# Kernel optimization log

Measured on AMD Instinct MI355X. Metric: run time of the kernel, lower is better.

The kernel has to match this reference:

```python
import jax, jax.numpy as jnp
import numpy as np


def setup_inputs() -> dict:
    key = jax.random.key(0)
    ks = jax.random.split(key, 13)
    B, T, D, H, E, C, S = 256, 64, 512, 512, 256, 6624, 26
    s = 0.05
    return {
        "batch_H": jax.random.normal(ks[0], (B, T, D), jnp.float32),
        "text": jax.random.randint(ks[1], (B, S), 0, C, jnp.int64),
        "W_i2h": jax.random.normal(ks[2], (H, D), jnp.float32) * s,
        "W_h2h": jax.random.normal(ks[3], (H, H), jnp.float32) * s,
        "b_h2h": jax.random.normal(ks[4], (H,), jnp.float32) * s,
        "w_score": jax.random.normal(ks[5], (H,), jnp.float32) * s,
        "W_ih": jax.random.normal(ks[6], (4 * H, D + E), jnp.float32) * s,
        "W_hh": jax.random.normal(ks[7], (4 * H, H), jnp.float32) * s,
        "b_ih": jax.random.normal(ks[8], (4 * H,), jnp.float32) * s,
        "b_hh": jax.random.normal(ks[9], (4 * H,), jnp.float32) * s,
        "emb": jax.random.normal(ks[10], (C, E), jnp.float32) * s,
        "W_gen": jax.random.normal(ks[11], (C, H), jnp.float32) * s,
        "b_gen": jax.random.normal(ks[12], (C,), jnp.float32) * s,
        "max_label_length": 25,
    }


def reference(batch_H, text, W_i2h, W_h2h, b_h2h, w_score, W_ih, W_hh,
              b_ih, b_hh, emb, W_gen, b_gen, max_label_length):
    B, T, D = batch_H.shape
    H = W_h2h.shape[0]
    num_steps = max_label_length + 1

    # i2h(batch_H) is constant across steps -> hoist out of the recurrence
    Hproj = jnp.einsum('btd,hd->bth', batch_H, W_i2h)  # [B,T,H]
    char_embs = emb[text[:, :num_steps]]               # [B,S,E]
    xs = jnp.transpose(char_embs, (1, 0, 2))           # [S,B,E]

    def step(carry, ce):
        h, c = carry
        hp = h @ W_h2h.T + b_h2h                       # [B,H]
        e = jnp.tanh(Hproj + hp[:, None, :]) @ w_score  # [B,T]
        alpha = jax.nn.softmax(e, axis=1)
        context = jnp.einsum('bt,btd->bd', alpha, batch_H)  # [B,D]
        x = jnp.concatenate([context, ce], axis=1)     # [B,D+E]
        gates = x @ W_ih.T + b_ih + h @ W_hh.T + b_hh  # [B,4H]
        i, f, g, o = jnp.split(gates, 4, axis=1)
        c_new = jax.nn.sigmoid(f) * c + jax.nn.sigmoid(i) * jnp.tanh(g)
        h_new = jax.nn.sigmoid(o) * jnp.tanh(c_new)
        return (h_new, c_new), h_new

    h0 = jnp.zeros((B, H), batch_H.dtype)
    c0 = jnp.zeros((B, H), batch_H.dtype)
    _, hs = jax.lax.scan(step, (h0, c0), xs)           # hs: [S,B,H]
    output_hiddens = jnp.transpose(hs, (1, 0, 2))      # [B,S,H]
    probs = output_hiddens @ W_gen.T + b_gen           # [B,S,C]
    return probs
```

## Files before the change

### kernel.cpp

```cpp
#include <hip/hip_runtime.h>

typedef unsigned short u16;
typedef unsigned int   u32;
typedef __attribute__((ext_vector_type(4))) float f32x4;
typedef __attribute__((ext_vector_type(8))) u16   u16x8;
typedef __attribute__((ext_vector_type(4))) u16   u16x4;
typedef __attribute__((ext_vector_type(4))) u32   u32x4;

__device__ __forceinline__ u16 f2bf(float x) {
  u32 u = __builtin_bit_cast(u32, x);
  u = (u + 0x7fffu + ((u >> 16) & 1u)) >> 16;
  return (u16)u;
}
__device__ __forceinline__ float bf2f(u16 h) {
  return __builtin_bit_cast(float, (u32)h << 16);
}
__device__ __forceinline__ float fast_sig(float x) { return 1.f / (1.f + __expf(-x)); }
__device__ __forceinline__ float fast_tanh(float x) {
  float e = __expf(2.f * x);
  return 1.f - 2.f / (e + 1.f);
}

__device__ __forceinline__ f32x4 mfma_bf16(u16x8 a, u16x8 b, f32x4 c) {
  asm volatile("v_mfma_f32_16x16x32_bf16 %0, %1, %2, %0" : "+v"(c) : "v"(a), "v"(b));
  return c;
}

__device__ __forceinline__ void gload_lds16(const void* g, void* l) {
  __builtin_amdgcn_global_load_lds(
      (__attribute__((address_space(1))) u32*)g,
      (__attribute__((address_space(3))) u32*)l, 16, 0, 0);
}

__device__ __forceinline__ void conv4(const float* __restrict__ s, u16* __restrict__ d, int i) {
  f32x4 v = *(const f32x4*)(s + i);
  u16x4 o;
  o.x = f2bf(v.x); o.y = f2bf(v.y); o.z = f2bf(v.z); o.w = f2bf(v.w);
  *(u16x4*)(d + i) = o;
}

__global__ __launch_bounds__(256) void k_prep(
    const float* __restrict__ batch_H, const float* __restrict__ W_i2h,
    const float* __restrict__ emb, const float* __restrict__ W_ih,
    const float* __restrict__ W_h2h, const float* __restrict__ W_hh,
    const float* __restrict__ W_gen, const float* __restrict__ b_ih,
    const float* __restrict__ b_hh,
    u16* __restrict__ bHb, u16* __restrict__ Wi2hb, u16* __restrict__ embb,
    u16* __restrict__ Wihb, u16* __restrict__ Whcatb, u16* __restrict__ Wgenb,
    float* __restrict__ biascat, u16* __restrict__ Acat, float* __restrict__ cst) {
  const u32 u = blockIdx.x * 256 + threadIdx.x;
  if (u < 2097152u) { conv4(batch_H, bHb, u * 4); return; }
  if (u < 2162688u) { conv4(W_i2h, Wi2hb, (u - 2097152u) * 4); return; }
  if (u < 2586624u) { conv4(emb, embb, (u - 2162688u) * 4); return; }
  if (u < 2979840u) { conv4(W_ih, Wihb, (u - 2586624u) * 4); return; }
  if (u < 3307520u) {
    int i = (u - 2979840u) * 4;
    int r = i >> 9, c = i & 511;
    const float* src = (r < 512) ? (W_h2h + (size_t)r * 512 + c)
                                 : (W_hh + (size_t)(r - 512) * 512 + c);
    f32x4 v = *(const f32x4*)src;
    u16x4 o;
    o.x = f2bf(v.x); o.y = f2bf(v.y); o.z = f2bf(v.z); o.w = f2bf(v.w);
    *(u16x4*)(Whcatb + i) = o;
    return;
  }
  if (u < 4159488u) {
    int i = (u - 3307520u) * 4;
    int r = i >> 9;
    if (r < 6624) conv4(W_gen, Wgenb, i);
    else *(u16x4*)(Wgenb + i) = (u16x4){0, 0, 0, 0};
    return;
  }
  if (u < 4160000u) {
    int j = (u - 4159488u) * 4;
    f32x4 a = *(const f32x4*)(b_ih + j), b = *(const f32x4*)(b_hh + j);
    f32x4 r = {a.x + b.x, a.y + b.y, a.z + b.z, a.w + b.w};
    *(f32x4*)(biascat + j) = r;
    return;
  }
  if (u < 4200960u) {
    *(u32x4*)((char*)Acat + (size_t)(u - 4160000u) * 16) = (u32x4){0, 0, 0, 0};
    return;
  }
  if (u < 4233728u) {
    *(u32x4*)((char*)cst + (size_t)(u - 4200960u) * 16) = (u32x4){0, 0, 0, 0};
    return;
  }
}

template <int BM, int BN, int WM, int WN, int OUT_MODE>
__global__ __launch_bounds__(256) void gemm_bt(const u16* __restrict__ A, int lda,
                                               const u16* __restrict__ B, int ldb,
                                               const float* __restrict__ bias,
                                               float* __restrict__ Cf, u16* __restrict__ Cb,
                                               int ldc, int Nreal, int K) {
  static_assert((BM / WM) * (BN / WN) == 4, "4 waves");
  constexpr int FM = WM / 16, FN = WN / 16;
  constexpr int NWC = BN / WN;
  constexpr int CHA = (BM * 4) / 256, CHB = (BN * 4) / 256;
  __shared__ __align__(16) u16 sA[BM * 32];
  __shared__ __align__(16) u16 sB[BN * 32];
  const int tid = threadIdx.x;
  const int lane = tid & 63, wave = tid >> 6;
  const int wr = wave / NWC, wc = wave % NWC;
  const int l15 = lane & 15, lhi = lane >> 4;
  const int m0 = blockIdx.y * BM, n0 = blockIdx.x * BN;

  f32x4 acc[FM][FN];
#pragma unroll
  for (int i = 0; i < FM; ++i)
#pragma unroll
    for (int j = 0; j < FN; ++j) acc[i][j] = 0.f;

  for (int k0 = 0; k0 < K; k0 += 32) {
    __syncthreads();
#pragma unroll
    for (int j = 0; j < CHA; ++j) {
      int idx = j * 256 + tid;
      int row = idx >> 2, cc = idx & 3;
      int c = cc ^ ((row >> 1) & 3);
      gload_lds16(A + (size_t)(m0 + row) * lda + (k0 + c * 8), sA + idx * 8);
    }
#pragma unroll
    for (int j = 0; j < CHB; ++j) {
      int idx = j * 256 + tid;
      int row = idx >> 2, cc = idx & 3;
      int c = cc ^ ((row >> 1) & 3);
      gload_lds16(B + (size_t)(n0 + row) * ldb + (k0 + c * 8), sB + idx * 8);
    }
    __syncthreads();

    u16x8 av[FM], bv[FN];
#pragma unroll
    for (int mi = 0; mi < FM; ++mi) {
      int row = wr * WM + mi * 16 + l15;
      int ch = row * 4 + (lhi ^ ((row >> 1) & 3));
      av[mi] = *(const u16x8*)(sA + ch * 8);
    }
#pragma unroll
    for (int ni = 0; ni < FN; ++ni) {
      int row = wc * WN + ni * 16 + l15;
      int ch = row * 4 + (lhi ^ ((row >> 1) & 3));
      bv[ni] = *(const u16x8*)(sB + ch * 8);
    }
#pragma unroll
    for (int mi = 0; mi < FM; ++mi)
#pragma unroll
      for (int ni = 0; ni < FN; ++ni) acc[mi][ni] = mfma_bf16(av[mi], bv[ni], acc[mi][ni]);
  }

  asm volatile("s_nop 7\ns_nop 7\ns_nop 7");

#pragma unroll
  for (int mi = 0; mi < FM; ++mi) {
#pragma unroll
    for (int ni = 0; ni < FN; ++ni) {
      int col = n0 + wc * WN + ni * 16 + l15;
      if (col < Nreal) {
        float bvv = (OUT_MODE == 1) ? bias[col] : 0.f;
#pragma unroll
        for (int r = 0; r < 4; ++r) {
          int row = m0 + wr * WM + mi * 16 + lhi * 4 + r;
          float v = acc[mi][ni][r] + bvv;
          if (OUT_MODE == 2)
            Cb[(size_t)row * ldc + col] = f2bf(v);
          else
            Cf[(size_t)row * ldc + col] = v;
        }
      }
    }
  }
}

__global__ __launch_bounds__(256) void kA_hpgh(const u16* __restrict__ Acat,
                                               const u16* __restrict__ Whcatb,
                                               const float* __restrict__ b_h2h,
                                               float* __restrict__ hpbuf,
                                               float* __restrict__ ghbuf) {
  __shared__ __align__(16) u16 sA[32 * 64];
  __shared__ __align__(16) u16 sB[128 * 64];
  const int tid = threadIdx.x;
  const int lane = tid & 63, wave = tid >> 6;
  const int wr = wave >> 1, wc = wave & 1;
  const int l15 = lane & 15, lhi = lane >> 4;
  const int b0 = ((int)blockIdx.x / 20) * 32, n0 = ((int)blockIdx.x % 20) * 128;

  f32x4 acc[4];
#pragma unroll
  for (int j = 0; j < 4; ++j) acc[j] = 0.f;

  for (int k0 = 0; k0 < 512; k0 += 64) {
    __syncthreads();
    {
      int row = tid >> 3, cc = tid & 7, c = cc ^ (row & 7);
      gload_lds16(Acat + (size_t)(b0 + row) * 1280 + 768 + k0 + c * 8, sA + tid * 8);
    }
#pragma unroll
    for (int j = 0; j < 4; ++j) {
      int idx = j * 256 + tid, row = idx >> 3, cc = idx & 7, c = cc ^ (row & 7);
      gload_lds16(Whcatb + (size_t)(n0 + row) * 512 + k0 + c * 8, sB + idx * 8);
    }
    __syncthreads();
#pragma unroll
    for (int ks = 0; ks < 2; ++ks) {
      u16x8 av, bv[4];
      {
        int row = wr * 16 + l15;
        int ch = row * 8 + ((ks * 4 + lhi) ^ (row & 7));
        av = *(const u16x8*)(sA + ch * 8);
      }
#pragma unroll
      for (int ni = 0; ni < 4; ++ni) {
        int row = wc * 64 + ni * 16 + l15;
        int ch = row * 8 + ((ks * 4 + lhi) ^ (row & 7));
        bv[ni] = *(const u16x8*)(sB + ch * 8);
      }
#pragma unroll
      for (int ni = 0; ni < 4; ++ni) acc[ni] = mfma_bf16(av, bv[ni], acc[ni]);
    }
  }
  asm volatile("s_nop 7\ns_nop 7\ns_nop 7");
#pragma unroll
  for (int ni = 0; ni < 4; ++ni) {
    int col = n0 + wc * 64 + ni * 16 + l15;
    int rowg = b0 + wr * 16 + lhi * 4;
    if (col < 512) {
      float bvv = b_h2h[col];
#pragma unroll
      for (int r = 0; r < 4; ++r)
        hpbuf[(size_t)(rowg + r) * 512 + col] = acc[ni][r] + bvv;
    } else {
#pragma unroll
      for (int r = 0; r < 4; ++r)
        ghbuf[(size_t)(rowg + r) * 2048 + col - 512] = acc[ni][r];
    }
  }
}

__global__ __launch_bounds__(256) void kB_attn(const u16* __restrict__ Hproj,
                                               const float* __restrict__ hpbuf,
                                               const float* __restrict__ wsc,
                                               const u16* __restrict__ bh,
                                               const u16* __restrict__ embb,
                                               const int* __restrict__ text, int step,
                                               u16* __restrict__ Acat) {
  const int b = blockIdx.x, tid = threadIdx.x;
  __shared__ float hpsp[528];
  __shared__ float wssp[528];
  __shared__ float es[64];

  {
    int j0 = tid * 2;
    hpsp[j0 + (j0 >> 5)] = hpbuf[(size_t)b * 512 + j0];
    hpsp[j0 + 1 + ((j0 + 1) >> 5)] = hpbuf[(size_t)b * 512 + j0 + 1];
    int pi = j0 + (j0 >> 5);
    wssp[pi] = wsc[j0];
    wssp[pi + 1] = wsc[j0 + 1];
  }
  __syncthreads();

  const int ch16 = tid & 15;
  const int hbase = ch16 * 33;
  const int hc = ch16 * 32;
  float hpr[32], wsr[32];
#pragma unroll
  for (int j = 0; j < 32; ++j) {
    hpr[j] = hpsp[hbase + j];
    wsr[j] = wssp[hbase + j];
  }
#pragma unroll
  for (int tg = 0; tg < 4; ++tg) {
    int t = tg * 16 + (tid >> 4);
    const u16* hr = Hproj + (size_t)(b * 64 + t) * 512 + hc;
    float s = 0.f;
#pragma unroll
    for (int jo = 0; jo < 32; jo += 8) {
      u16x8 hv = *(const u16x8*)(hr + jo);
#pragma unroll
      for (int j = 0; j < 8; ++j) {
        float x = bf2f(hv[j]) + hpr[jo + j];
        s += fast_tanh(x) * wsr[jo + j];
      }
    }
#pragma unroll
    for (int off = 8; off; off >>= 1) s += __shfl_xor(s, off, 16);
    if (ch16 == 0) es[t] = s;
  }
  __syncthreads();
  if (tid < 64) {
    float v = es[tid];
    float m = v;
#pragma unroll
    for (int o = 32; o; o >>= 1) m = fmaxf(m, __shfl_xor(m, o, 64));
    float p = __expf(v - m);
    float su = p;
#pragma unroll
    for (int o = 32; o; o >>= 1) su += __shfl_xor(su, o, 64);
    es[tid] = p / su;
  }
  __syncthreads();
  const u16* base = bh + (size_t)b * 32768 + tid * 2;
  float c0 = 0.f, c1 = 0.f;
#pragma unroll 8
  for (int t = 0; t < 64; ++t) {
    u32 w = *(const u32*)(base + t * 512);
    float a = es[t];
    c0 = fmaf(a, bf2f((u16)(w & 0xffffu)), c0);
    c1 = fmaf(a, bf2f((u16)(w >> 16)), c1);
  }
  u32 pk = (u32)f2bf(c0) | ((u32)f2bf(c1) << 16);
  *(u32*)(Acat + (size_t)b * 1280 + tid * 2) = pk;
  int ci = text[b * 26 + step];
  Acat[(size_t)b * 1280 + 512 + tid] = embb[(size_t)ci * 256 + tid];
}

__global__ __launch_bounds__(256) void kC_gates_lstm(const u16* __restrict__ Acat_ro,
                                                     const u16* __restrict__ Wihb,
                                                     const float* __restrict__ biascat,
                                                     const float* __restrict__ ghbuf,
                                                     float* __restrict__ cst,
                                                     u16* __restrict__ Acat,
                                                     u16* __restrict__ hsb, int step) {
  __shared__ __align__(16) char smem[20480];
  u16* sA = (u16*)smem;
  u16* sB = (u16*)(smem + 4096);
  const int tid = threadIdx.x;
  const int lane = tid & 63, wave = tid >> 6;
  const int wr = wave >> 1, wc = wave & 1;
  const int l15 = lane & 15, lhi = lane >> 4;
  const int jt = blockIdx.x;
  const int b0 = blockIdx.y * 32;

  f32x4 acc[4];
#pragma unroll
  for (int j = 0; j < 4; ++j) acc[j] = 0.f;

  for (int k0 = 0; k0 < 768; k0 += 64) {
    __syncthreads();
    {
      int row = tid >> 3, cc = tid & 7, c = cc ^ (row & 7);
      gload_lds16(Acat_ro + (size_t)(b0 + row) * 1280 + k0 + c * 8, sA + tid * 8);
    }
#pragma unroll
    for (int j = 0; j < 4; ++j) {
      int idx = j * 256 + tid, row = idx >> 3, cc = idx & 7, c = cc ^ (row & 7);
      int grow = (row >> 5) * 512 + jt * 32 + (row & 31);
      gload_lds16(Wihb + (size_t)grow * 768 + k0 + c * 8, sB + idx * 8);
    }
    __syncthreads();

#pragma unroll
    for (int ks = 0; ks < 2; ++ks) {
      u16x8 av, bv[4];
      {
        int row = wr * 16 + l15;
        int ch = row * 8 + ((ks * 4 + lhi) ^ (row & 7));
        av = *(const u16x8*)(sA + ch * 8);
      }
#pragma unroll
      for (int ni = 0; ni < 4; ++ni) {
        int row = wc * 64 + ni * 16 + l15;
        int ch = row * 8 + ((ks * 4 + lhi) ^ (row & 7));
        bv[ni] = *(const u16x8*)(sB + ch * 8);
      }
#pragma unroll
      for (int ni = 0; ni < 4; ++ni) acc[ni] = mfma_bf16(av, bv[ni], acc[ni]);
    }
  }

  asm volatile("s_nop 7\ns_nop 7\ns_nop 7");
  __syncthreads();
  float (*gsm)[132] = (float(*)[132])smem;
#pragma unroll
  for (int ni = 0; ni < 4; ++ni) {
    int col = wc * 64 + ni * 16 + l15;
    int row = wr * 16 + lhi * 4;
#pragma unroll
    for (int r = 0; r < 4; ++r) gsm[row + r][col] = acc[ni][r];
  }
  __syncthreads();

  {
    const int bl = tid >> 3, jl0 = (tid & 7) * 4;
    const int b = b0 + bl;
    const int jg0 = jt * 32 + jl0;
    const float* gh = ghbuf + (size_t)b * 2048;
    float cn[4];
    u16 hb[4];
#pragma unroll
    for (int q = 0; q < 4; ++q) {
      int jl = jl0 + q, j = jg0 + q;
      float gi = gsm[bl][jl]      + gh[j]        + biascat[j];
      float gf = gsm[bl][32 + jl] + gh[512 + j]  + biascat[512 + j];
      float gg = gsm[bl][64 + jl] + gh[1024 + j] + biascat[1024 + j];
      float go = gsm[bl][96 + jl] + gh[1536 + j] + biascat[1536 + j];
      float c = fast_sig(gf) * cst[(size_t)b * 512 + j] + fast_sig(gi) * fast_tanh(gg);
      cn[q] = c;
      hb[q] = f2bf(fast_sig(go) * fast_tanh(c));
    }
    *(f32x4*)(cst + (size_t)b * 512 + jg0) = *(f32x4*)cn;
    *(u16x4*)(Acat + (size_t)b * 1280 + 768 + jg0) = *(u16x4*)hb;
    *(u16x4*)(hsb + (size_t)(b * 26 + step) * 512 + jg0) = *(u16x4*)hb;
  }
}

extern "C" void kernel_launch(void* const* d_in, const int* in_sizes, int n_in,
                              void* d_out, int out_size, void* d_ws, size_t ws_size,
                              hipStream_t stream) {
  const float* batch_H = (const float*)d_in[0];
  const int*   text    = (const int*)d_in[1];
  const float* W_i2h   = (const float*)d_in[2];
  const float* W_h2h   = (const float*)d_in[3];
  const float* b_h2h   = (const float*)d_in[4];
  const float* w_score = (const float*)d_in[5];
  const float* W_ih    = (const float*)d_in[6];
  const float* W_hh    = (const float*)d_in[7];
  const float* b_ih    = (const float*)d_in[8];
  const float* b_hh    = (const float*)d_in[9];
  const float* emb     = (const float*)d_in[10];
  const float* W_gen   = (const float*)d_in[11];
  const float* b_gen   = (const float*)d_in[12];
  float* out = (float*)d_out;

  u16* bHb   = (u16*)d_out;
  u16* Hproj = bHb + 8388608;

  char* w = (char*)d_ws;
  auto alloc = [&](size_t bytes) {
    char* p = w;
    w += (bytes + 255) & ~(size_t)255;
    return p;
  };
  u16*   Wi2hb   = (u16*)alloc(512ull * 512 * 2);
  u16*   Whcatb  = (u16*)alloc(2560ull * 512 * 2);
  u16*   Wihb    = (u16*)alloc(2048ull * 768 * 2);
  u16*   Wgenb   = (u16*)alloc(6656ull * 512 * 2);
  u16*   embb    = (u16*)alloc(6624ull * 256 * 2);
  float* biascat = (float*)alloc(2048ull * 4);
  u16*   Acat    = (u16*)alloc(256ull * 1280 * 2);
  float* cst     = (float*)alloc(256ull * 512 * 4);
  float* hpbuf   = (float*)alloc(256ull * 512 * 4);
  float* ghbuf   = (float*)alloc(256ull * 2048 * 4);
  u16*   hsb     = (u16*)alloc(6656ull * 512 * 2);

  k_prep<<<16538, 256, 0, stream>>>(batch_H, W_i2h, emb, W_ih, W_h2h, W_hh, W_gen,
                                    b_ih, b_hh, bHb, Wi2hb, embb, Wihb, Whcatb,
                                    Wgenb, biascat, Acat, cst);

  gemm_bt<128, 128, 64, 64, 2><<<dim3(4, 128), 256, 0, stream>>>(
      bHb, 512, Wi2hb, 512, nullptr, nullptr, Hproj, 512, 512, 512);

  for (int s = 0; s < 26; ++s) {
    kA_hpgh<<<160, 256, 0, stream>>>(Acat, Whcatb, b_h2h, hpbuf, ghbuf);
    kB_attn<<<256, 256, 0, stream>>>(Hproj, hpbuf, w_score, bHb, embb, text, s, Acat);
    kC_gates_lstm<<<dim3(16, 8), 256, 0, stream>>>(Acat, Wihb, biascat, ghbuf, cst,
                                                   Acat, hsb, s);
  }

  gemm_bt<128, 128, 64, 64, 1><<<dim3(52, 52), 256, 0, stream>>>(
      hsb, 512, Wgenb, 512, b_gen, out, nullptr, 6624, 6624, 512);

  (void)in_sizes; (void)n_in; (void)out_size; (void)ws_size;
}
```

Measured before the change: 902.1 us.

## Precompute embedding-to-gate table and split W_ih; widen K tiles in step kernels

```diff
diff --git a/kernel.cpp b/kernel.cpp
--- a/kernel.cpp
+++ b/kernel.cpp
@@ -46,15 +46,37 @@
     const float* __restrict__ W_gen, const float* __restrict__ b_ih,
     const float* __restrict__ b_hh,
     u16* __restrict__ bHb, u16* __restrict__ Wi2hb, u16* __restrict__ embb,
-    u16* __restrict__ Wihb, u16* __restrict__ Whcatb, u16* __restrict__ Wgenb,
-    float* __restrict__ biascat, u16* __restrict__ Acat, float* __restrict__ cst) {
+    u16* __restrict__ Wctxb, u16* __restrict__ Wceb, u16* __restrict__ Whcatb,
+    u16* __restrict__ Wgenb, float* __restrict__ biascat,
+    u16* __restrict__ hb, float* __restrict__ cst) {
   const u32 u = blockIdx.x * 256 + threadIdx.x;
   if (u < 2097152u) { conv4(batch_H, bHb, u * 4); return; }
   if (u < 2162688u) { conv4(W_i2h, Wi2hb, (u - 2097152u) * 4); return; }
   if (u < 2586624u) { conv4(emb, embb, (u - 2162688u) * 4); return; }
-  if (u < 2979840u) { conv4(W_ih, Wihb, (u - 2586624u) * 4); return; }
-  if (u < 3307520u) {
-    int i = (u - 2979840u) * 4;
+  if (u < 2588672u) {
+    *(u16x4*)(embb + 1695744u + (u - 2586624u) * 4) = (u16x4){0, 0, 0, 0};
+    return;
+  }
+  if (u < 2850816u) {
+    int i = (u - 2588672u) * 4;
+    int r = i >> 9, c = i & 511;
+    f32x4 v = *(const f32x4*)(W_ih + (size_t)r * 768 + c);
+    u16x4 o;
+    o.x = f2bf(v.x); o.y = f2bf(v.y); o.z = f2bf(v.z); o.w = f2bf(v.w);
+    *(u16x4*)(Wctxb + i) = o;
+    return;
+  }
+  if (u < 2981888u) {
+    int i = (u - 2850816u) * 4;
+    int r = i >> 8, c = i & 255;
+    f32x4 v = *(const f32x4*)(W_ih + (size_t)r * 768 + 512 + c);
+    u16x4 o;
+    o.x = f2bf(v.x); o.y = f2bf(v.y); o.z = f2bf(v.z); o.w = f2bf(v.w);
+    *(u16x4*)(Wceb + i) = o;
+    return;
+  }
+  if (u < 3309568u) {
+    int i = (u - 2981888u) * 4;
     int r = i >> 9, c = i & 511;
     const float* src = (r < 512) ? (W_h2h + (size_t)r * 512 + c)
                                  : (W_hh + (size_t)(r - 512) * 512 + c);
@@ -64,26 +86,26 @@
     *(u16x4*)(Whcatb + i) = o;
     return;
   }
-  if (u < 4159488u) {
-    int i = (u - 3307520u) * 4;
+  if (u < 4161536u) {
+    int i = (u - 3309568u) * 4;
     int r = i >> 9;
     if (r < 6624) conv4(W_gen, Wgenb, i);
     else *(u16x4*)(Wgenb + i) = (u16x4){0, 0, 0, 0};
     return;
   }
-  if (u < 4160000u) {
-    int j = (u - 4159488u) * 4;
+  if (u < 4162048u) {
+    int j = (u - 4161536u) * 4;
     f32x4 a = *(const f32x4*)(b_ih + j), b = *(const f32x4*)(b_hh + j);
     f32x4 r = {a.x + b.x, a.y + b.y, a.z + b.z, a.w + b.w};
     *(f32x4*)(biascat + j) = r;
     return;
   }
-  if (u < 4200960u) {
-    *(u32x4*)((char*)Acat + (size_t)(u - 4160000u) * 16) = (u32x4){0, 0, 0, 0};
-    return;
-  }
-  if (u < 4233728u) {
-    *(u32x4*)((char*)cst + (size_t)(u - 4200960u) * 16) = (u32x4){0, 0, 0, 0};
+  if (u < 4178432u) {
+    *(u32x4*)((char*)hb + (size_t)(u - 4162048u) * 16) = (u32x4){0, 0, 0, 0};
+    return;
+  }
+  if (u < 4211200u) {
+    *(u32x4*)((char*)cst + (size_t)(u - 4178432u) * 16) = (u32x4){0, 0, 0, 0};
     return;
   }
 }
@@ -172,13 +194,13 @@
   }
 }
 
-__global__ __launch_bounds__(256) void kA_hpgh(const u16* __restrict__ Acat,
+__global__ __launch_bounds__(256) void kA_hpgh(const u16* __restrict__ hb,
                                                const u16* __restrict__ Whcatb,
                                                const float* __restrict__ b_h2h,
                                                float* __restrict__ hpbuf,
                                                float* __restrict__ ghbuf) {
-  __shared__ __align__(16) u16 sA[32 * 64];
-  __shared__ __align__(16) u16 sB[128 * 64];
+  __shared__ __align__(16) u16 sA[32 * 128];
+  __shared__ __align__(16) u16 sB[128 * 128];
   const int tid = threadIdx.x;
   const int lane = tid & 63, wave = tid >> 6;
   const int wr = wave >> 1, wc = wave & 1;
@@ -189,30 +211,31 @@
 #pragma unroll
   for (int j = 0; j < 4; ++j) acc[j] = 0.f;
 
-  for (int k0 = 0; k0 < 512; k0 += 64) {
-    __syncthreads();
-    {
-      int row = tid >> 3, cc = tid & 7, c = cc ^ (row & 7);
-      gload_lds16(Acat + (size_t)(b0 + row) * 1280 + 768 + k0 + c * 8, sA + tid * 8);
-    }
-#pragma unroll
-    for (int j = 0; j < 4; ++j) {
-      int idx = j * 256 + tid, row = idx >> 3, cc = idx & 7, c = cc ^ (row & 7);
+  for (int k0 = 0; k0 < 512; k0 += 128) {
+    __syncthreads();
+#pragma unroll
+    for (int j = 0; j < 2; ++j) {
+      int idx = j * 256 + tid, row = idx >> 4, cc = idx & 15, c = cc ^ (row & 15);
+      gload_lds16(hb + (size_t)(b0 + row) * 512 + k0 + c * 8, sA + idx * 8);
+    }
+#pragma unroll
+    for (int j = 0; j < 8; ++j) {
+      int idx = j * 256 + tid, row = idx >> 4, cc = idx & 15, c = cc ^ (row & 15);
       gload_lds16(Whcatb + (size_t)(n0 + row) * 512 + k0 + c * 8, sB + idx * 8);
     }
     __syncthreads();
 #pragma unroll
-    for (int ks = 0; ks < 2; ++ks) {
+    for (int ks = 0; ks < 4; ++ks) {
       u16x8 av, bv[4];
       {
         int row = wr * 16 + l15;
-        int ch = row * 8 + ((ks * 4 + lhi) ^ (row & 7));
+        int ch = row * 16 + ((ks * 4 + lhi) ^ (row & 15));
         av = *(const u16x8*)(sA + ch * 8);
       }
 #pragma unroll
       for (int ni = 0; ni < 4; ++ni) {
         int row = wc * 64 + ni * 16 + l15;
-        int ch = row * 8 + ((ks * 4 + lhi) ^ (row & 7));
+        int ch = row * 16 + ((ks * 4 + lhi) ^ (row & 15));
         bv[ni] = *(const u16x8*)(sB + ch * 8);
       }
 #pragma unroll
@@ -241,9 +264,7 @@
                                                const float* __restrict__ hpbuf,
                                                const float* __restrict__ wsc,
                                                const u16* __restrict__ bh,
-                                               const u16* __restrict__ embb,
-                                               const int* __restrict__ text, int step,
-                                               u16* __restrict__ Acat) {
+                                               u16* __restrict__ ctxb) {
   const int b = blockIdx.x, tid = threadIdx.x;
   __shared__ float hpsp[528];
   __shared__ float wssp[528];
@@ -309,21 +330,20 @@
     c1 = fmaf(a, bf2f((u16)(w >> 16)), c1);
   }
   u32 pk = (u32)f2bf(c0) | ((u32)f2bf(c1) << 16);
-  *(u32*)(Acat + (size_t)b * 1280 + tid * 2) = pk;
-  int ci = text[b * 26 + step];
-  Acat[(size_t)b * 1280 + 512 + tid] = embb[(size_t)ci * 256 + tid];
-}
-
-__global__ __launch_bounds__(256) void kC_gates_lstm(const u16* __restrict__ Acat_ro,
-                                                     const u16* __restrict__ Wihb,
-                                                     const float* __restrict__ biascat,
+  *(u32*)(ctxb + (size_t)b * 512 + tid * 2) = pk;
+}
+
+__global__ __launch_bounds__(256) void kC_gates_lstm(const u16* __restrict__ ctxb,
+                                                     const u16* __restrict__ Wctxb,
+                                                     const float* __restrict__ E2G,
                                                      const float* __restrict__ ghbuf,
+                                                     const int* __restrict__ text,
                                                      float* __restrict__ cst,
-                                                     u16* __restrict__ Acat,
+                                                     u16* __restrict__ hb,
                                                      u16* __restrict__ hsb, int step) {
-  __shared__ __align__(16) char smem[20480];
+  __shared__ __align__(16) char smem[40960];
   u16* sA = (u16*)smem;
-  u16* sB = (u16*)(smem + 4096);
+  u16* sB = (u16*)(smem + 8192);
   const int tid = threadIdx.x;
   const int lane = tid & 63, wave = tid >> 6;
   const int wr = wave >> 1, wc = wave & 1;
@@ -335,32 +355,33 @@
 #pragma unroll
   for (int j = 0; j < 4; ++j) acc[j] = 0.f;
 
-  for (int k0 = 0; k0 < 768; k0 += 64) {
-    __syncthreads();
-    {
-      int row = tid >> 3, cc = tid & 7, c = cc ^ (row & 7);
-      gload_lds16(Acat_ro + (size_t)(b0 + row) * 1280 + k0 + c * 8, sA + tid * 8);
-    }
-#pragma unroll
-    for (int j = 0; j < 4; ++j) {
-      int idx = j * 256 + tid, row = idx >> 3, cc = idx & 7, c = cc ^ (row & 7);
+  for (int k0 = 0; k0 < 512; k0 += 128) {
+    __syncthreads();
+#pragma unroll
+    for (int j = 0; j < 2; ++j) {
+      int idx = j * 256 + tid, row = idx >> 4, cc = idx & 15, c = cc ^ (row & 15);
+      gload_lds16(ctxb + (size_t)(b0 + row) * 512 + k0 + c * 8, sA + idx * 8);
+    }
+#pragma unroll
+    for (int j = 0; j < 8; ++j) {
+      int idx = j * 256 + tid, row = idx >> 4, cc = idx & 15, c = cc ^ (row & 15);
       int grow = (row >> 5) * 512 + jt * 32 + (row & 31);
-      gload_lds16(Wihb + (size_t)grow * 768 + k0 + c * 8, sB + idx * 8);
-    }
-    __syncthreads();
-
-#pragma unroll
-    for (int ks = 0; ks < 2; ++ks) {
+      gload_lds16(Wctxb + (size_t)grow * 512 + k0 + c * 8, sB + idx * 8);
+    }
+    __syncthreads();
+
+#pragma unroll
+    for (int ks = 0; ks < 4; ++ks) {
       u16x8 av, bv[4];
       {
         int row = wr * 16 + l15;
-        int ch = row * 8 + ((ks * 4 + lhi) ^ (row & 7));
+        int ch = row * 16 + ((ks * 4 + lhi) ^ (row & 15));
         av = *(const u16x8*)(sA + ch * 8);
       }
 #pragma unroll
       for (int ni = 0; ni < 4; ++ni) {
         int row = wc * 64 + ni * 16 + l15;
-        int ch = row * 8 + ((ks * 4 + lhi) ^ (row & 7));
+        int ch = row * 16 + ((ks * 4 + lhi) ^ (row & 15));
         bv[ni] = *(const u16x8*)(sB + ch * 8);
       }
 #pragma unroll
@@ -384,23 +405,25 @@
     const int bl = tid >> 3, jl0 = (tid & 7) * 4;
     const int b = b0 + bl;
     const int jg0 = jt * 32 + jl0;
+    const int ci = text[b * 26 + step];
     const float* gh = ghbuf + (size_t)b * 2048;
+    const float* ge = E2G + (size_t)ci * 2048;
     float cn[4];
-    u16 hb[4];
+    u16 hbv[4];
 #pragma unroll
     for (int q = 0; q < 4; ++q) {
       int jl = jl0 + q, j = jg0 + q;
-      float gi = gsm[bl][jl]      + gh[j]        + biascat[j];
-      float gf = gsm[bl][32 + jl] + gh[512 + j]  + biascat[512 + j];
-      float gg = gsm[bl][64 + jl] + gh[1024 + j] + biascat[1024 + j];
-      float go = gsm[bl][96 + jl] + gh[1536 + j] + biascat[1536 + j];
+      float gi = gsm[bl][jl]      + gh[j]        + ge[j];
+      float gf = gsm[bl][32 + jl] + gh[512 + j]  + ge[512 + j];
+      float gg = gsm[bl][64 + jl] + gh[1024 + j] + ge[1024 + j];
+      float go = gsm[bl][96 + jl] + gh[1536 + j] + ge[1536 + j];
       float c = fast_sig(gf) * cst[(size_t)b * 512 + j] + fast_sig(gi) * fast_tanh(gg);
       cn[q] = c;
-      hb[q] = f2bf(fast_sig(go) * fast_tanh(c));
+      hbv[q] = f2bf(fast_sig(go) * fast_tanh(c));
     }
     *(f32x4*)(cst + (size_t)b * 512 + jg0) = *(f32x4*)cn;
-    *(u16x4*)(Acat + (size_t)b * 1280 + 768 + jg0) = *(u16x4*)hb;
-    *(u16x4*)(hsb + (size_t)(b * 26 + step) * 512 + jg0) = *(u16x4*)hb;
+    *(u16x4*)(hb + (size_t)b * 512 + jg0) = *(u16x4*)hbv;
+    *(u16x4*)(hsb + (size_t)(b * 26 + step) * 512 + jg0) = *(u16x4*)hbv;
   }
 }
 
@@ -433,28 +456,34 @@
   };
   u16*   Wi2hb   = (u16*)alloc(512ull * 512 * 2);
   u16*   Whcatb  = (u16*)alloc(2560ull * 512 * 2);
-  u16*   Wihb    = (u16*)alloc(2048ull * 768 * 2);
+  u16*   Wctxb   = (u16*)alloc(2048ull * 512 * 2);
+  u16*   Wceb    = (u16*)alloc(2048ull * 256 * 2);
   u16*   Wgenb   = (u16*)alloc(6656ull * 512 * 2);
-  u16*   embb    = (u16*)alloc(6624ull * 256 * 2);
+  u16*   embb    = (u16*)alloc(6656ull * 256 * 2);
   float* biascat = (float*)alloc(2048ull * 4);
-  u16*   Acat    = (u16*)alloc(256ull * 1280 * 2);
+  u16*   ctxb    = (u16*)alloc(256ull * 512 * 2);
+  u16*   hb      = (u16*)alloc(256ull * 512 * 2);
   float* cst     = (float*)alloc(256ull * 512 * 4);
   float* hpbuf   = (float*)alloc(256ull * 512 * 4);
   float* ghbuf   = (float*)alloc(256ull * 2048 * 4);
   u16*   hsb     = (u16*)alloc(6656ull * 512 * 2);
-
-  k_prep<<<16538, 256, 0, stream>>>(batch_H, W_i2h, emb, W_ih, W_h2h, W_hh, W_gen,
-                                    b_ih, b_hh, bHb, Wi2hb, embb, Wihb, Whcatb,
-                                    Wgenb, biascat, Acat, cst);
+  float* E2G     = (float*)alloc(6656ull * 2048 * 4);
+
+  k_prep<<<16450, 256, 0, stream>>>(batch_H, W_i2h, emb, W_ih, W_h2h, W_hh, W_gen,
+                                    b_ih, b_hh, bHb, Wi2hb, embb, Wctxb, Wceb,
+                                    Whcatb, Wgenb, biascat, hb, cst);
 
   gemm_bt<128, 128, 64, 64, 2><<<dim3(4, 128), 256, 0, stream>>>(
       bHb, 512, Wi2hb, 512, nullptr, nullptr, Hproj, 512, 512, 512);
 
+  gemm_bt<128, 128, 64, 64, 1><<<dim3(16, 52), 256, 0, stream>>>(
+      embb, 256, Wceb, 256, biascat, E2G, nullptr, 2048, 2048, 256);
+
   for (int s = 0; s < 26; ++s) {
-    kA_hpgh<<<160, 256, 0, stream>>>(Acat, Whcatb, b_h2h, hpbuf, ghbuf);
-    kB_attn<<<256, 256, 0, stream>>>(Hproj, hpbuf, w_score, bHb, embb, text, s, Acat);
-    kC_gates_lstm<<<dim3(16, 8), 256, 0, stream>>>(Acat, Wihb, biascat, ghbuf, cst,
-                                                   Acat, hsb, s);
+    kA_hpgh<<<160, 256, 0, stream>>>(hb, Whcatb, b_h2h, hpbuf, ghbuf);
+    kB_attn<<<256, 256, 0, stream>>>(Hproj, hpbuf, w_score, bHb, ctxb);
+    kC_gates_lstm<<<dim3(16, 8), 256, 0, stream>>>(ctxb, Wctxb, E2G, ghbuf, text,
+                                                   cst, hb, hsb, s);
   }
 
   gemm_bt<128, 128, 64, 64, 1><<<dim3(52, 52), 256, 0, stream>>>(
```

Result: faster. 823.7 us (-8.7%).
